# Kernel optimization log

Measured on AMD Instinct MI355X. Metric: run time of the kernel, lower is better.

## Reference

```python
import jax, jax.numpy as jnp
import numpy as np

EPS = 1e-6


def _feature_map(x):
    # elu(x) + 1
    return jax.nn.elu(x) + 1.0


def _causal_dot(Qb, Kb, V):
    """Causal linear attention numerator for 3 stacked branches.
    Qb, Kb: [3, N, L, H, D]; V: [N, L, H, Dv] -> out [3, N, L, H, Dv].
    out[b,n,l,h,:] = sum_{s<=l} (Qb[b,n,l,h,:] . Kb[b,n,s,h,:]) V[n,s,h,:]
    computed with an O(L) recurrent scan over cumulative KV outer products.
    """
    Qs = jnp.moveaxis(Qb, 2, 0)  # [L, 3, N, H, D]
    Ks = jnp.moveaxis(Kb, 2, 0)  # [L, 3, N, H, D]
    Vs = jnp.moveaxis(V, 1, 0)   # [L, N, H, Dv]
    B, N, _, H, D = Qb.shape
    Dv = V.shape[-1]
    S0 = jnp.zeros((B, N, H, D, Dv), dtype=Qb.dtype)

    def step(S, inp):
        q, k, v = inp  # q,k: [3,N,H,D], v: [N,H,Dv]
        S = S + k[..., :, None] * v[None, :, :, None, :]
        o = jnp.einsum('bnhi,bnhij->bnhj', q, S)
        return S, o

    _, out = jax.lax.scan(step, S0, (Qs, Ks, Vs))  # out: [L,3,N,H,Dv]
    return jnp.moveaxis(out, 0, 2)  # [3,N,L,H,Dv]


def setup_inputs() -> dict:
    key = jax.random.key(0)
    ks = jax.random.split(key, 5)
    N, L, H, D = 4, 2048, 8, 128
    return {
        'queries': jax.random.normal(ks[0], (N, L, H, D), dtype=jnp.float32),
        'q2': jax.random.normal(ks[1], (N, L, H, D), dtype=jnp.float32),
        'keys': jax.random.normal(ks[2], (N, L, H, D), dtype=jnp.float32),
        'values': jax.random.normal(ks[3], (N, L, H, D), dtype=jnp.float32),
        'key_lengths': jnp.ones((N, L), dtype=jnp.float32),
        'omega': jax.random.normal(ks[4], (H, D, D), dtype=jnp.float32),
    }


def reference(queries, q2, keys, values, key_lengths, omega):
    N, L, H, D = queries.shape
    Q = _feature_map(queries)                       # [N,L,H,D]
    K = _feature_map(keys) * key_lengths[:, :, None, None]

    # Delta[n,l,h,i] = l/L for all n,h,i -> projection through omega reduces to
    # (l/L) * sum_i omega[h,i,j], same math as einsum('nlhi,hij->nlhj', Delta, omega).
    delta = (jnp.arange(L, dtype=queries.dtype) / L)        # [L]
    t = delta[:, None, None] * jnp.sum(omega, axis=1)[None]  # [L,H,D]
    sin_t, cos_t = jnp.sin(t), jnp.cos(t)
    s2, c2, sc = sin_t ** 2, cos_t ** 2, sin_t * cos_t       # [L,H,D] each

    # Q_term = sin(phi(q2))^2 * feature_map(queries)
    q2_proj = jnp.einsum('nlhi,hij->nlhj', q2, omega)
    Q_term = (jnp.sin(q2_proj) ** 2) * Q                     # [N,L,H,D]

    # Branch trig weights: Q gets [sin^2, cos^2, sin*cos], K gets [cos^2, sin^2, sin*cos]
    wq = jnp.stack([s2, c2, sc])[:, None]  # [3,1,L,H,D]
    wk = jnp.stack([c2, s2, sc])[:, None]
    Qb = Q_term[None] * wq                 # [3,N,L,H,D]
    Kb = K[None] * wk                      # [3,N,L,H,D]

    # Denominator terms Z_b = <Q_b[l], cumsum_{s<=l} K_b[s]>
    Kcum = jnp.cumsum(Kb, axis=2)
    Z = jnp.einsum('bnlhi,bnlhi->bnlh', Qb, Kcum)   # [3,N,L,H]

    Vb = _causal_dot(Qb, Kb, values)                # [3,N,L,H,D]

    numerator = Vb[0] + Vb[1] - 2.0 * Vb[2]
    denominator = Z[0] + Z[1] - 2.0 * Z[2] + EPS
    return numerator / denominator[:, :, :, None]
```

## Files before the change

kernel.cpp:

```cpp
#include <hip/hip_runtime.h>


typedef float f32x4 __attribute__((ext_vector_type(4)));
typedef short s16x8 __attribute__((ext_vector_type(8)));
typedef unsigned short u16;

static constexpr int    Ln   = 2048;
static constexpr size_t NHLD = (size_t)32 * 2048 * 128;
static constexpr size_t KSB  = (size_t)32 * 16 * 128;

__device__ __forceinline__ float b2f(u16 s) {
  union { unsigned u; float f; } x; x.u = ((unsigned)s) << 16; return x.f;
}
__device__ __forceinline__ u16 f2b(float f) {
  union { float f; unsigned u; } x; x.f = f;
  unsigned r = x.u + 0x7fffu + ((x.u >> 16) & 1u);
  return (u16)(r >> 16);
}
__device__ __forceinline__ s16x8 pack8(f32x4 a, f32x4 b) {
  s16x8 r;
  r[0] = (short)f2b(a[0]); r[1] = (short)f2b(a[1]); r[2] = (short)f2b(a[2]); r[3] = (short)f2b(a[3]);
  r[4] = (short)f2b(b[0]); r[5] = (short)f2b(b[1]); r[6] = (short)f2b(b[2]); r[7] = (short)f2b(b[3]);
  return r;
}

__global__ __launch_bounds__(256) void k_omega(const float* __restrict__ om,
                                               u16* __restrict__ wt, float* __restrict__ osum) {
  __shared__ alignas(16) u16 T[128][136];
  int h = blockIdx.x, t = threadIdx.x;
  for (int idx = t; idx < 128 * 32; idx += 256) {
    int i = idx >> 5, cs = (idx & 31) << 2;
    f32x4 vv = *(const f32x4*)(om + ((size_t)(h * 128 + i)) * 128 + cs);
    T[i][cs + 0] = f2b(vv[0]); T[i][cs + 1] = f2b(vv[1]);
    T[i][cs + 2] = f2b(vv[2]); T[i][cs + 3] = f2b(vv[3]);
  }
  if (t < 128) {
    float acc = 0.f;
    for (int i = 0; i < 128; i++) acc += om[((size_t)(h * 128 + i)) * 128 + t];
    osum[h * 128 + t] = acc;
  }
  __syncthreads();
  {
    int j = t >> 1, lh = (t & 1) << 6;
    s16x8* dst = (s16x8*)(wt + ((size_t)(h * 128 + j)) * 128 + lh);
    for (int u = 0; u < 8; u++) {
      s16x8 pv;
#pragma unroll
      for (int e = 0; e < 8; e++) pv[e] = (short)T[lh + u * 8 + e][j];
      dst[u] = pv;
    }
  }
}

__global__ __launch_bounds__(256) void k_kvfeat(const float* __restrict__ kg, const float* __restrict__ vg,
                                                const float* __restrict__ klg, const float* __restrict__ osum,
                                                u16* __restrict__ kb3, u16* __restrict__ kbt3,
                                                u16* __restrict__ vt) {
  __shared__ alignas(16) u16 Bu[4][32][136];
  __shared__ float osb[128];
  int bid = blockIdx.x, t = threadIdx.x;
  int lt = bid & 15, h = (bid >> 4) & 7, n = bid >> 7;
  int l0 = lt << 7, nh = (n << 3) + h;
  const float invL = 1.0f / 2048.0f;
  if (t < 128) osb[t] = osum[h * 128 + t];
  for (int strip = 0; strip < 4; strip++) {
    int ls0 = strip << 5;
    __syncthreads();
    for (int idx = t; idx < 1024; idx += 256) {
      int rr = idx >> 5, cs = (idx & 31) << 2;
      int l = l0 + ls0 + rr;
      size_t gb = (((size_t)(n * Ln + l) * 8 + h) << 7) + cs;
      f32x4 kv = *(const f32x4*)(kg + gb);
      f32x4 vv = *(const f32x4*)(vg + gb);
      float klv = klg[n * Ln + l];
      float tb = (float)l * invL;
#pragma unroll
      for (int e = 0; e < 4; e++) {
        int i = cs + e;
        float kf = (kv[e] > 0.f ? kv[e] + 1.f : __expf(kv[e])) * klv;
        float tt = tb * osb[i];
        float s, c; __sincosf(tt, &s, &c);
        Bu[0][rr][i] = f2b(kf * c * c);
        Bu[1][rr][i] = f2b(kf * s * s);
        Bu[2][rr][i] = f2b(kf * s * c);
        Bu[3][rr][i] = f2b(vv[e]);
      }
    }
    __syncthreads();
    for (int idx = t; idx < 2560; idx += 256) {
      if (idx < 1024) {
        int arr = idx >> 8, rem = idx & 255, i = rem >> 1, hf = rem & 1;
        int lc = hf << 4;
        u16 tmp[16];
#pragma unroll
        for (int u = 0; u < 16; u++) tmp[u] = Bu[arr][lc + u][i];
        u16* dst; size_t db;
        if (arr < 3) { dst = kbt3; db = ((size_t)((arr * 32 + nh) * 128 + i)) * Ln + (l0 + ls0 + lc); }
        else         { dst = vt;   db = ((size_t)(nh * 128 + i)) * Ln + (l0 + ls0 + lc); }
        s16x8 p0, p1;
#pragma unroll
        for (int e = 0; e < 8; e++) { p0[e] = (short)tmp[e]; p1[e] = (short)tmp[8 + e]; }
        *(s16x8*)(dst + db) = p0;
        *(s16x8*)(dst + db + 8) = p1;
      } else {
        int r2 = idx - 1024, arr = r2 >> 9, rem = r2 & 511, rr = rem >> 4, g = (rem & 15) << 3;
        s16x8 pv = *(const s16x8*)&Bu[arr][rr][g];
        *(s16x8*)(kb3 + (size_t)arr * NHLD + ((size_t)nh * Ln + l0 + ls0 + rr) * 128 + g) = pv;
      }
    }
  }
}

__global__ __launch_bounds__(512, 4) void p1a(const u16* __restrict__ vtg, const u16* __restrict__ kbt3,
                                              u16* __restrict__ sct, float* __restrict__ ksum) {
  __shared__ alignas(16) u16 B[128][136];
  int bid = blockIdx.x, t = threadIdx.x;
  int c = bid & 15, h = (bid >> 4) & 7, n = (bid >> 7) & 3, b = bid >> 9;
  int l0 = c << 7, nh = (n << 3) + h, bnh = b * 32 + nh;
  int lane = t & 63, quad = lane >> 4, nl = lane & 15, w = t >> 6;
  for (int idx = t; idx < 2048; idx += 512) {
    int i = idx >> 4, cs = (idx & 15) << 3;
    *(s16x8*)&B[i][cs] = *(const s16x8*)(kbt3 + ((size_t)(bnh * 128 + i)) * Ln + l0 + cs);
  }
  __syncthreads();
  f32x4 z4 = {0.f, 0.f, 0.f, 0.f};
  f32x4 acc[8];
#pragma unroll
  for (int i = 0; i < 8; i++) acc[i] = z4;
  int arow = (w << 4) + nl;
  for (int ks = 0; ks < 4; ks++) {
    int k0 = (ks << 5) + (quad << 3);
    s16x8 av = *(const s16x8*)(vtg + ((size_t)(nh * 128 + arow)) * Ln + l0 + k0);
#pragma unroll
    for (int ct = 0; ct < 8; ct++) {
      s16x8 bv = *(const s16x8*)&B[(ct << 4) + nl][k0];
      acc[ct] = __builtin_amdgcn_mfma_f32_16x16x32_bf16(av, bv, acc[ct], 0, 0, 0);
    }
  }
  if (t < 128) {
    float s = 0.f;
#pragma unroll 4
    for (int g = 0; g < 128; g += 8) {
      s16x8 v = *(const s16x8*)&B[t][g];
#pragma unroll
      for (int e = 0; e < 8; e++) s += b2f((u16)v[e]);
    }
    ksum[(size_t)(bnh * 16 + c) * 128 + t] = s;
  }
  __syncthreads();
  {
    int lbase = (w << 4) + (quad << 2);
#pragma unroll
    for (int ct = 0; ct < 8; ct++) {
      int i = (ct << 4) + nl;
#pragma unroll
      for (int r = 0; r < 4; r++) B[lbase + r][i] = f2b(acc[ct][r]);
    }
  }
  __syncthreads();
  size_t sbase = ((size_t)(bnh * 16 + c)) << 14;
  for (int idx = t; idx < 2048; idx += 512) {
    int jr = idx >> 4, g = (idx & 15) << 3;
    *(s16x8*)(sct + sbase + ((size_t)jr << 7) + g) = *(const s16x8*)&B[jr][g];
  }
}

__global__ __launch_bounds__(256) void p1b(u16* __restrict__ sct, float* __restrict__ ksum) {
  int bid = blockIdx.x, t = threadIdx.x;
  if (bid < 768) {
    int tid = bid * 256 + t;
    int bnh = tid >> 11, rem = tid & 2047;
    size_t base = ((size_t)bnh << 18) + ((size_t)rem << 3);
    float acc[8] = {0.f, 0.f, 0.f, 0.f, 0.f, 0.f, 0.f, 0.f};
    for (int c = 0; c < 16; c++) {
      size_t a = base + ((size_t)c << 14);
      s16x8 v = *(const s16x8*)(sct + a);
      s16x8 o;
#pragma unroll
      for (int e = 0; e < 8; e++) { o[e] = (short)f2b(acc[e]); acc[e] += b2f((u16)v[e]); }
      *(s16x8*)(sct + a) = o;
    }
  } else {
    int m2 = (bid - 768) * 256 + t;
    int i = m2 & 127, bnh = m2 >> 7;
    size_t base = (size_t)bnh * 2048 + i;
    float acc = 0.f;
    for (int c = 0; c < 16; c++) {
      size_t a = base + (size_t)c * 128;
      float v = ksum[a];
      ksum[a] = acc;
      acc += v;
    }
  }
}

__global__ __launch_bounds__(256, 2) void k_qfeat(const float* __restrict__ q2g, const float* __restrict__ qg,
                                                  const u16* __restrict__ wt, const float* __restrict__ osum,
                                                  const float* __restrict__ kspre,
                                                  u16* __restrict__ qb3, float* __restrict__ zintg) {
  __shared__ alignas(16) u16 B[128][136];
  __shared__ float osb[128];
  int bid = blockIdx.x, t = threadIdx.x;
  int m = bid & 31, h = (bid >> 5) & 7, n = bid >> 8;
  int l0 = m << 6, c = m >> 1, nh = (n << 3) + h;
  if (t < 128) osb[t] = osum[h * 128 + t];
  for (int idx = t; idx < 2048; idx += 256) {
    int j = idx >> 4, cs = (idx & 15) << 3;
    *(s16x8*)&B[j][cs] = *(const s16x8*)(wt + ((size_t)(h * 128 + j)) * 128 + cs);
  }
  __syncthreads();
  int lane = t & 63, quad = lane >> 4, nl = lane & 15, w = t >> 6;
  f32x4 z4 = {0.f, 0.f, 0.f, 0.f};
  f32x4 acc[8];
#pragma unroll
  for (int i = 0; i < 8; i++) acc[i] = z4;
  int arow = l0 + (w << 4) + nl;
  for (int ks = 0; ks < 4; ks++) {
    int k0 = (ks << 5) + (quad << 3);
    const float* ap = q2g + (((size_t)(n * Ln + arow) * 8 + h) << 7) + k0;
    s16x8 av = pack8(*(const f32x4*)ap, *(const f32x4*)(ap + 4));
#pragma unroll
    for (int ct = 0; ct < 8; ct++) {
      s16x8 bv = *(const s16x8*)&B[(ct << 4) + nl][k0];
      acc[ct] = __builtin_amdgcn_mfma_f32_16x16x32_bf16(av, bv, acc[ct], 0, 0, 0);
    }
  }
  __syncthreads();
  {
    int lbase = (w << 4) + (quad << 2);
#pragma unroll
    for (int ct = 0; ct < 8; ct++) {
      int j = (ct << 4) + nl;
#pragma unroll
      for (int r = 0; r < 4; r++) {
        float sp = __sinf(acc[ct][r]);
        B[lbase + r][j] = f2b(sp * sp);
      }
    }
  }
  __syncthreads();
  const float invL = 1.0f / 2048.0f;
  for (int idx = t; idx < 1024; idx += 256) {
    int l = idx >> 4, j0 = (idx & 15) << 3, gl = l0 + l;
    s16x8 s2v = *(const s16x8*)&B[l][j0];
    const float* qp = qg + (((size_t)(n * Ln + gl) * 8 + h) << 7) + j0;
    f32x4 qa = *(const f32x4*)qp, qbv = *(const f32x4*)(qp + 4);
    size_t kbb = ((size_t)nh * 16 + c) * 128 + j0;
    f32x4 kp0a = *(const f32x4*)(kspre + kbb),           kp0b = *(const f32x4*)(kspre + kbb + 4);
    f32x4 kp1a = *(const f32x4*)(kspre + kbb + KSB),     kp1b = *(const f32x4*)(kspre + kbb + KSB + 4);
    f32x4 kp2a = *(const f32x4*)(kspre + kbb + 2 * KSB), kp2b = *(const f32x4*)(kspre + kbb + 2 * KSB + 4);
    s16x8 o0, o1, o2;
    float z = 0.f;
    float tb = (float)gl * invL;
#pragma unroll
    for (int e = 0; e < 8; e++) {
      float s2p = b2f((u16)s2v[e]);
      float qv = (e < 4) ? qa[e] : qbv[e - 4];
      float f = qv > 0.f ? qv + 1.f : __expf(qv);
      float Qt = s2p * f;
      float tt = tb * osb[j0 + e];
      float s, cc; __sincosf(tt, &s, &cc);
      float v0 = Qt * s * s, v1 = Qt * cc * cc, v2 = -2.f * Qt * s * cc;
      float k0v = (e < 4) ? kp0a[e] : kp0b[e - 4];
      float k1v = (e < 4) ? kp1a[e] : kp1b[e - 4];
      float k2v = (e < 4) ? kp2a[e] : kp2b[e - 4];
      z += v0 * k0v + v1 * k1v + v2 * k2v;
      o0[e] = (short)f2b(v0); o1[e] = (short)f2b(v1); o2[e] = (short)f2b(v2);
    }
    size_t base = ((size_t)nh * Ln + gl) * 128 + j0;
    *(s16x8*)(qb3 + base)            = o0;
    *(s16x8*)(qb3 + base + NHLD)     = o1;
    *(s16x8*)(qb3 + base + 2 * NHLD) = o2;
    z += __shfl_xor(z, 1); z += __shfl_xor(z, 2);
    z += __shfl_xor(z, 4); z += __shfl_xor(z, 8);
    if (nl == 0) zintg[(size_t)nh * Ln + gl] = z;
  }
}

__global__ __launch_bounds__(512, 4) void p3(const u16* __restrict__ qb3, const u16* __restrict__ kb3,
                                             const u16* __restrict__ vtg, const u16* __restrict__ sct,
                                             const float* __restrict__ zintg, float* __restrict__ outg) {
  __shared__ union {
    struct { alignas(16) u16 B[128][136]; alignas(16) u16 P[128][136]; } s;
    alignas(16) float O[128][132];
  } sm;
  int bid = blockIdx.x, t = threadIdx.x;
  int c = bid & 15, h = (bid >> 4) & 7, n = bid >> 7;
  int l0c = c << 7, nh = (n << 3) + h;
  int lane = t & 63, quad = lane >> 4, nl = lane & 15, w = t >> 6;
  f32x4 z4 = {0.f, 0.f, 0.f, 0.f};
  f32x4 accP[8], accO[8];
#pragma unroll
  for (int i = 0; i < 8; i++) { accP[i] = z4; accO[i] = z4; }
  int arow = l0c + (w << 4) + nl;
  for (int b = 0; b < 3; b++) {
    int bnh = b * 32 + nh;
    __syncthreads();
    for (int idx = t; idx < 2048; idx += 512) {
      int s = idx >> 4, cs = (idx & 15) << 3;
      *(s16x8*)&sm.s.B[s][cs] = *(const s16x8*)(kb3 + (((size_t)bnh * Ln + l0c + s) << 7) + cs);
    }
    __syncthreads();
    s16x8 av[4];
#pragma unroll
    for (int ks = 0; ks < 4; ks++)
      av[ks] = *(const s16x8*)(qb3 + (((size_t)bnh * Ln + arow) << 7) + (ks << 5) + (quad << 3));
    for (int ks = 0; ks < 4; ks++) {
      int k0 = (ks << 5) + (quad << 3);
#pragma unroll
      for (int ct = 0; ct < 8; ct++) {
        s16x8 bv = *(const s16x8*)&sm.s.B[(ct << 4) + nl][k0];
        accP[ct] = __builtin_amdgcn_mfma_f32_16x16x32_bf16(av[ks], bv, accP[ct], 0, 0, 0);
      }
    }
    __syncthreads();
    size_t sbase = ((size_t)(bnh * 16 + c)) << 14;
    for (int idx = t; idx < 2048; idx += 512) {
      int j = idx >> 4, cs = (idx & 15) << 3;
      *(s16x8*)&sm.s.B[j][cs] = *(const s16x8*)(sct + sbase + ((size_t)j << 7) + cs);
    }
    __syncthreads();
    for (int ks = 0; ks < 4; ks++) {
      int k0 = (ks << 5) + (quad << 3);
#pragma unroll
      for (int ct = 0; ct < 8; ct++) {
        s16x8 bv = *(const s16x8*)&sm.s.B[(ct << 4) + nl][k0];
        accO[ct] = __builtin_amdgcn_mfma_f32_16x16x32_bf16(av[ks], bv, accO[ct], 0, 0, 0);
      }
    }
  }
  __syncthreads();
  float zP[4] = {0.f, 0.f, 0.f, 0.f};
  int lbase = (w << 4) + (quad << 2);
#pragma unroll
  for (int ct = 0; ct < 8; ct++) {
    int ss = (ct << 4) + nl;
#pragma unroll
    for (int r = 0; r < 4; r++) {
      int lr = lbase + r;
      float pv = (ss <= lr) ? accP[ct][r] : 0.f;
      zP[r] += pv;
      sm.s.P[lr][ss] = f2b(pv);
    }
  }
#pragma unroll
  for (int mteam = 1; mteam <= 8; mteam <<= 1) {
#pragma unroll
    for (int r = 0; r < 4; r++) zP[r] += __shfl_xor(zP[r], mteam);
  }
  for (int idx = t; idx < 2048; idx += 512) {
    int j = idx >> 4, cs = (idx & 15) << 3;
    *(s16x8*)&sm.s.B[j][cs] = *(const s16x8*)(vtg + ((size_t)(nh * 128 + j)) * Ln + l0c + cs);
  }
  float zf[4];
#pragma unroll
  for (int r = 0; r < 4; r++)
    zf[r] = zintg[(size_t)nh * Ln + l0c + lbase + r] + zP[r] + 1e-6f;
  __syncthreads();
  for (int ks = 0; ks < 4; ks++) {
    int k0 = (ks << 5) + (quad << 3);
    s16x8 pav = *(const s16x8*)&sm.s.P[(w << 4) + nl][k0];
#pragma unroll
    for (int ct = 0; ct < 8; ct++) {
      s16x8 vv = *(const s16x8*)&sm.s.B[(ct << 4) + nl][k0];
      accO[ct] = __builtin_amdgcn_mfma_f32_16x16x32_bf16(pav, vv, accO[ct], 0, 0, 0);
    }
  }
  __syncthreads();
#pragma unroll
  for (int ct = 0; ct < 8; ct++) {
    int j = (ct << 4) + nl;
#pragma unroll
    for (int r = 0; r < 4; r++) sm.O[lbase + r][j] = accO[ct][r] / zf[r];
  }
  __syncthreads();
  for (int idx = t; idx < 4096; idx += 512) {
    int l = idx >> 5, g = (idx & 31) << 2;
    *(f32x4*)(outg + (((size_t)(n * Ln + l0c + l) * 8 + h) << 7) + g) = *(const f32x4*)&sm.O[l][g];
  }
}

extern "C" void kernel_launch(void* const* d_in, const int* in_sizes, int n_in,
                              void* d_out, int out_size, void* d_ws, size_t ws_size,
                              hipStream_t stream) {
  (void)in_sizes; (void)n_in; (void)out_size; (void)ws_size;
  const float* q   = (const float*)d_in[0];
  const float* q2  = (const float*)d_in[1];
  const float* kk  = (const float*)d_in[2];
  const float* vv  = (const float*)d_in[3];
  const float* kl  = (const float*)d_in[4];
  const float* om  = (const float*)d_in[5];
  float* out = (float*)d_out;

  u16* W     = (u16*)d_ws;
  u16* qb3   = W;
  u16* kb3   = W + 3 * NHLD;
  u16* kbt3  = W + 6 * NHLD;
  u16* vt    = W + 9 * NHLD;
  u16* sct   = W + 10 * NHLD;
  u16* wt    = W + 13 * NHLD;
  float* ks  = (float*)(W + 13 * NHLD + 131072);
  float* osm = ks + 196608;
  float* zin = osm + 1024;

  k_omega <<<8,    256, 0, stream>>>(om, wt, osm);
  k_kvfeat<<<512,  256, 0, stream>>>(kk, vv, kl, osm, kb3, kbt3, vt);
  p1a     <<<1536, 512, 0, stream>>>(vt, kbt3, sct, ks);
  p1b     <<<816,  256, 0, stream>>>(sct, ks);
  k_qfeat <<<1024, 256, 0, stream>>>(q2, q, wt, osm, ks, qb3, zin);
  p3      <<<512,  512, 0, stream>>>(qb3, kb3, vt, sct, zin, out);
}
```

Baseline: 293.0 us.

## Restructure kvfeat, qfeat and p3 to shrink LDS and change block shapes

k_kvfeat now runs twice as many blocks, each covering 64 rows in two passes through a smaller odd-padded LDS buffer. It writes the row-major kb3 directly from registers and does the transposes with wider stores. k_qfeat switches to 512-thread blocks covering 128 rows. p3 shares one LDS tile for K, S, P, reads V fragments straight from global memory, and writes output through a half-size LDS staging buffer. The goal is lower LDS use and higher occupancy, at the cost of uncoalesced global V reads in p3 and extra sin/cos work recomputed across passes in kvfeat.

New measurement: 304.2 us. +3.8%, slower.

```diff
diff --git a/kernel.cpp b/kernel.cpp
--- a/kernel.cpp
+++ b/kernel.cpp
@@ -3,6 +3,7 @@
 
 typedef float f32x4 __attribute__((ext_vector_type(4)));
 typedef short s16x8 __attribute__((ext_vector_type(8)));
+typedef short s16x4 __attribute__((ext_vector_type(4)));
 typedef unsigned short u16;
 
 static constexpr int    Ln   = 2048;
@@ -56,56 +57,66 @@
                                                 const float* __restrict__ klg, const float* __restrict__ osum,
                                                 u16* __restrict__ kb3, u16* __restrict__ kbt3,
                                                 u16* __restrict__ vt) {
-  __shared__ alignas(16) u16 Bu[4][32][136];
+  __shared__ u16 U[2][64][137];
   __shared__ float osb[128];
   int bid = blockIdx.x, t = threadIdx.x;
-  int lt = bid & 15, h = (bid >> 4) & 7, n = bid >> 7;
-  int l0 = lt << 7, nh = (n << 3) + h;
+  int ls = bid & 31, h = (bid >> 5) & 7, n = bid >> 8;
+  int l0 = ls << 6, nh = (n << 3) + h;
   const float invL = 1.0f / 2048.0f;
   if (t < 128) osb[t] = osum[h * 128 + t];
-  for (int strip = 0; strip < 4; strip++) {
-    int ls0 = strip << 5;
-    __syncthreads();
-    for (int idx = t; idx < 1024; idx += 256) {
+  for (int p = 0; p < 2; p++) {
+    __syncthreads();
+    for (int idx = t; idx < 2048; idx += 256) {
       int rr = idx >> 5, cs = (idx & 31) << 2;
-      int l = l0 + ls0 + rr;
+      int l = l0 + rr;
       size_t gb = (((size_t)(n * Ln + l) * 8 + h) << 7) + cs;
       f32x4 kv = *(const f32x4*)(kg + gb);
-      f32x4 vv = *(const f32x4*)(vg + gb);
       float klv = klg[n * Ln + l];
       float tb = (float)l * invL;
-#pragma unroll
-      for (int e = 0; e < 4; e++) {
-        int i = cs + e;
-        float kf = (kv[e] > 0.f ? kv[e] + 1.f : __expf(kv[e])) * klv;
-        float tt = tb * osb[i];
-        float s, c; __sincosf(tt, &s, &c);
-        Bu[0][rr][i] = f2b(kf * c * c);
-        Bu[1][rr][i] = f2b(kf * s * s);
-        Bu[2][rr][i] = f2b(kf * s * c);
-        Bu[3][rr][i] = f2b(vv[e]);
-      }
-    }
-    __syncthreads();
-    for (int idx = t; idx < 2560; idx += 256) {
-      if (idx < 1024) {
-        int arr = idx >> 8, rem = idx & 255, i = rem >> 1, hf = rem & 1;
-        int lc = hf << 4;
-        u16 tmp[16];
-#pragma unroll
-        for (int u = 0; u < 16; u++) tmp[u] = Bu[arr][lc + u][i];
-        u16* dst; size_t db;
-        if (arr < 3) { dst = kbt3; db = ((size_t)((arr * 32 + nh) * 128 + i)) * Ln + (l0 + ls0 + lc); }
-        else         { dst = vt;   db = ((size_t)(nh * 128 + i)) * Ln + (l0 + ls0 + lc); }
-        s16x8 p0, p1;
-#pragma unroll
-        for (int e = 0; e < 8; e++) { p0[e] = (short)tmp[e]; p1[e] = (short)tmp[8 + e]; }
-        *(s16x8*)(dst + db) = p0;
-        *(s16x8*)(dst + db + 8) = p1;
+      if (p == 0) {
+        s16x4 o0, o1;
+#pragma unroll
+        for (int e = 0; e < 4; e++) {
+          float kf = (kv[e] > 0.f ? kv[e] + 1.f : __expf(kv[e])) * klv;
+          float s, c; __sincosf(tb * osb[cs + e], &s, &c);
+          u16 b0 = f2b(kf * c * c), b1 = f2b(kf * s * s);
+          o0[e] = (short)b0; o1[e] = (short)b1;
+          U[0][rr][cs + e] = b0; U[1][rr][cs + e] = b1;
+        }
+        size_t nb = ((size_t)nh * Ln + l) * 128 + cs;
+        *(s16x4*)(kb3 + nb) = o0;
+        *(s16x4*)(kb3 + nb + NHLD) = o1;
       } else {
-        int r2 = idx - 1024, arr = r2 >> 9, rem = r2 & 511, rr = rem >> 4, g = (rem & 15) << 3;
-        s16x8 pv = *(const s16x8*)&Bu[arr][rr][g];
-        *(s16x8*)(kb3 + (size_t)arr * NHLD + ((size_t)nh * Ln + l0 + ls0 + rr) * 128 + g) = pv;
+        f32x4 vv = *(const f32x4*)(vg + gb);
+        s16x4 o2;
+#pragma unroll
+        for (int e = 0; e < 4; e++) {
+          float kf = (kv[e] > 0.f ? kv[e] + 1.f : __expf(kv[e])) * klv;
+          float s, c; __sincosf(tb * osb[cs + e], &s, &c);
+          u16 b2 = f2b(kf * s * c);
+          o2[e] = (short)b2;
+          U[0][rr][cs + e] = b2; U[1][rr][cs + e] = f2b(vv[e]);
+        }
+        *(s16x4*)(kb3 + ((size_t)nh * Ln + l) * 128 + cs + 2 * NHLD) = o2;
+      }
+    }
+    __syncthreads();
+    for (int idx = t; idx < 512; idx += 256) {
+      int a = idx >> 8, rem = idx & 255, i = rem >> 1, hf = rem & 1;
+      int s0 = hf << 5;
+      u16 tmp[32];
+#pragma unroll
+      for (int u = 0; u < 32; u++) tmp[u] = U[a][s0 + u][i];
+      int arr = p * 2 + a;
+      u16* dst; size_t db;
+      if (arr < 3) { dst = kbt3; db = ((size_t)((arr * 32 + nh) * 128 + i)) * Ln + l0 + s0; }
+      else         { dst = vt;   db = ((size_t)(nh * 128 + i)) * Ln + l0 + s0; }
+#pragma unroll
+      for (int g = 0; g < 4; g++) {
+        s16x8 pv;
+#pragma unroll
+        for (int e = 0; e < 8; e++) pv[e] = (short)tmp[g * 8 + e];
+        *(s16x8*)(dst + db + g * 8) = pv;
       }
     }
   }
@@ -194,17 +205,17 @@
   }
 }
 
-__global__ __launch_bounds__(256, 2) void k_qfeat(const float* __restrict__ q2g, const float* __restrict__ qg,
+__global__ __launch_bounds__(512, 4) void k_qfeat(const float* __restrict__ q2g, const float* __restrict__ qg,
                                                   const u16* __restrict__ wt, const float* __restrict__ osum,
                                                   const float* __restrict__ kspre,
                                                   u16* __restrict__ qb3, float* __restrict__ zintg) {
   __shared__ alignas(16) u16 B[128][136];
   __shared__ float osb[128];
   int bid = blockIdx.x, t = threadIdx.x;
-  int m = bid & 31, h = (bid >> 5) & 7, n = bid >> 8;
-  int l0 = m << 6, c = m >> 1, nh = (n << 3) + h;
+  int mb = bid & 15, h = (bid >> 4) & 7, n = bid >> 7;
+  int l0 = mb << 7, c = mb, nh = (n << 3) + h;
   if (t < 128) osb[t] = osum[h * 128 + t];
-  for (int idx = t; idx < 2048; idx += 256) {
+  for (int idx = t; idx < 2048; idx += 512) {
     int j = idx >> 4, cs = (idx & 15) << 3;
     *(s16x8*)&B[j][cs] = *(const s16x8*)(wt + ((size_t)(h * 128 + j)) * 128 + cs);
   }
@@ -240,7 +251,7 @@
   }
   __syncthreads();
   const float invL = 1.0f / 2048.0f;
-  for (int idx = t; idx < 1024; idx += 256) {
+  for (int idx = t; idx < 2048; idx += 512) {
     int l = idx >> 4, j0 = (idx & 15) << 3, gl = l0 + l;
     s16x8 s2v = *(const s16x8*)&B[l][j0];
     const float* qp = qg + (((size_t)(n * Ln + gl) * 8 + h) << 7) + j0;
@@ -281,8 +292,8 @@
                                              const u16* __restrict__ vtg, const u16* __restrict__ sct,
                                              const float* __restrict__ zintg, float* __restrict__ outg) {
   __shared__ union {
-    struct { alignas(16) u16 B[128][136]; alignas(16) u16 P[128][136]; } s;
-    alignas(16) float O[128][132];
+    alignas(16) u16 T[128][136];
+    alignas(16) float Oh[64][132];
   } sm;
   int bid = blockIdx.x, t = threadIdx.x;
   int c = bid & 15, h = (bid >> 4) & 7, n = bid >> 7;
@@ -298,7 +309,7 @@
     __syncthreads();
     for (int idx = t; idx < 2048; idx += 512) {
       int s = idx >> 4, cs = (idx & 15) << 3;
-      *(s16x8*)&sm.s.B[s][cs] = *(const s16x8*)(kb3 + (((size_t)bnh * Ln + l0c + s) << 7) + cs);
+      *(s16x8*)&sm.T[s][cs] = *(const s16x8*)(kb3 + (((size_t)bnh * Ln + l0c + s) << 7) + cs);
     }
     __syncthreads();
     s16x8 av[4];
@@ -309,7 +320,7 @@
       int k0 = (ks << 5) + (quad << 3);
 #pragma unroll
       for (int ct = 0; ct < 8; ct++) {
-        s16x8 bv = *(const s16x8*)&sm.s.B[(ct << 4) + nl][k0];
+        s16x8 bv = *(const s16x8*)&sm.T[(ct << 4) + nl][k0];
         accP[ct] = __builtin_amdgcn_mfma_f32_16x16x32_bf16(av[ks], bv, accP[ct], 0, 0, 0);
       }
     }
@@ -317,14 +328,14 @@
     size_t sbase = ((size_t)(bnh * 16 + c)) << 14;
     for (int idx = t; idx < 2048; idx += 512) {
       int j = idx >> 4, cs = (idx & 15) << 3;
-      *(s16x8*)&sm.s.B[j][cs] = *(const s16x8*)(sct + sbase + ((size_t)j << 7) + cs);
+      *(s16x8*)&sm.T[j][cs] = *(const s16x8*)(sct + sbase + ((size_t)j << 7) + cs);
     }
     __syncthreads();
     for (int ks = 0; ks < 4; ks++) {
       int k0 = (ks << 5) + (quad << 3);
 #pragma unroll
       for (int ct = 0; ct < 8; ct++) {
-        s16x8 bv = *(const s16x8*)&sm.s.B[(ct << 4) + nl][k0];
+        s16x8 bv = *(const s16x8*)&sm.T[(ct << 4) + nl][k0];
         accO[ct] = __builtin_amdgcn_mfma_f32_16x16x32_bf16(av[ks], bv, accO[ct], 0, 0, 0);
       }
     }
@@ -340,17 +351,13 @@
       int lr = lbase + r;
       float pv = (ss <= lr) ? accP[ct][r] : 0.f;
       zP[r] += pv;
-      sm.s.P[lr][ss] = f2b(pv);
+      sm.T[lr][ss] = f2b(pv);
     }
   }
 #pragma unroll
   for (int mteam = 1; mteam <= 8; mteam <<= 1) {
 #pragma unroll
     for (int r = 0; r < 4; r++) zP[r] += __shfl_xor(zP[r], mteam);
-  }
-  for (int idx = t; idx < 2048; idx += 512) {
-    int j = idx >> 4, cs = (idx & 15) << 3;
-    *(s16x8*)&sm.s.B[j][cs] = *(const s16x8*)(vtg + ((size_t)(nh * 128 + j)) * Ln + l0c + cs);
   }
   float zf[4];
 #pragma unroll
@@ -359,24 +366,30 @@
   __syncthreads();
   for (int ks = 0; ks < 4; ks++) {
     int k0 = (ks << 5) + (quad << 3);
-    s16x8 pav = *(const s16x8*)&sm.s.P[(w << 4) + nl][k0];
+    s16x8 pav = *(const s16x8*)&sm.T[(w << 4) + nl][k0];
 #pragma unroll
     for (int ct = 0; ct < 8; ct++) {
-      s16x8 vv = *(const s16x8*)&sm.s.B[(ct << 4) + nl][k0];
+      s16x8 vv = *(const s16x8*)(vtg + ((size_t)(nh * 128 + (ct << 4) + nl)) * Ln + l0c + k0);
       accO[ct] = __builtin_amdgcn_mfma_f32_16x16x32_bf16(pav, vv, accO[ct], 0, 0, 0);
     }
   }
-  __syncthreads();
-#pragma unroll
-  for (int ct = 0; ct < 8; ct++) {
-    int j = (ct << 4) + nl;
-#pragma unroll
-    for (int r = 0; r < 4; r++) sm.O[lbase + r][j] = accO[ct][r] / zf[r];
-  }
-  __syncthreads();
-  for (int idx = t; idx < 4096; idx += 512) {
-    int l = idx >> 5, g = (idx & 31) << 2;
-    *(f32x4*)(outg + (((size_t)(n * Ln + l0c + l) * 8 + h) << 7) + g) = *(const f32x4*)&sm.O[l][g];
+  for (int hb = 0; hb < 2; hb++) {
+    __syncthreads();
+    if ((lbase >> 6) == hb) {
+      int lb = lbase & 63;
+#pragma unroll
+      for (int ct = 0; ct < 8; ct++) {
+        int j = (ct << 4) + nl;
+#pragma unroll
+        for (int r = 0; r < 4; r++) sm.Oh[lb + r][j] = accO[ct][r] / zf[r];
+      }
+    }
+    __syncthreads();
+    for (int idx = t; idx < 2048; idx += 512) {
+      int l = idx >> 5, g = (idx & 31) << 2;
+      *(f32x4*)(outg + (((size_t)(n * Ln + l0c + (hb << 6) + l) * 8 + h) << 7) + g) =
+          *(const f32x4*)&sm.Oh[l][g];
+    }
   }
 }
 
@@ -404,9 +417,9 @@
   float* zin = osm + 1024;
 
   k_omega <<<8,    256, 0, stream>>>(om, wt, osm);
-  k_kvfeat<<<512,  256, 0, stream>>>(kk, vv, kl, osm, kb3, kbt3, vt);
+  k_kvfeat<<<1024, 256, 0, stream>>>(kk, vv, kl, osm, kb3, kbt3, vt);
   p1a     <<<1536, 512, 0, stream>>>(vt, kbt3, sct, ks);
   p1b     <<<816,  256, 0, stream>>>(sct, ks);
-  k_qfeat <<<1024, 256, 0, stream>>>(q2, q, wt, osm, ks, qb3, zin);
+  k_qfeat <<<512,  512, 0, stream>>>(q2, q, wt, osm, ks, qb3, zin);
   p3      <<<512,  512, 0, stream>>>(qb3, kb3, vt, sct, zin, out);
 }
```
